# Optimization experiments

Measured on AMD Instinct MI355X. Metric: run time of the kernel, lower is better.

## Reference

```python
import jax, jax.numpy as jnp
import numpy as np

N_STEPS = 20
ALPHA, BETA = 0.9, 0.8  # synaptic / membrane decay (unused given zero carried state, kept for clarity)


def _lcn_spiking_layer(h, knn, w, b):
    """h: [N, d_in]; knn: [d_out, K] indices into d_in; w: [d_out, K]; b: [1, d_out].
    Gather K neighbors per output node, weight, reduce, then snntorch Synaptic
    update with zero carried state (the source never stores returned syn/mem):
      syn = ALPHA*0 + I = I ; reset = (prev_mem > thr) = 0 ; mem = BETA*0 + syn - 0 = I
    and the layer output is mem (the source keeps the 3rd return value)."""
    g = h[:, knn]                                  # [N, d_out, K] irregular gather
    cur = jnp.sum(g * w[None, :, :], axis=2) + b   # [N, d_out]
    syn = ALPHA * jnp.zeros_like(cur) + cur
    mem = BETA * jnp.zeros_like(cur) + syn         # reset term is zero
    return mem


def setup_inputs() -> dict:
    key = jax.random.key(0)
    B, T, IN_DIM, K, OUT = 32, N_STEPS, 14400, 25, 2
    dims = [7200, 3600, 1800, 900, 450]
    ks = jax.random.split(key, 13)
    inp = {"x": jax.random.normal(ks[0], (B, T, IN_DIM), dtype=jnp.float32)}
    prev = IN_DIM
    for i, d in enumerate(dims):
        inp[f"w{i}"] = jax.random.normal(ks[1 + i], (d, K), dtype=jnp.float32) * (2.0 / K) ** 0.5
        inp[f"b{i}"] = jnp.zeros((1, d), dtype=jnp.float32)
        inp[f"knn{i}"] = jax.random.randint(ks[6 + i], (d, K), 0, prev)
        prev = d
    inp["Wfc"] = jax.random.normal(ks[11], (dims[-1], OUT), dtype=jnp.float32) * (1.0 / dims[-1]) ** 0.5
    inp["bfc"] = jnp.zeros((OUT,), dtype=jnp.float32)
    return inp


def reference(x, w0, w1, w2, w3, w4, b0, b1, b2, b3, b4, Wfc, bfc,
              knn0, knn1, knn2, knn3, knn4):
    # Source loops over 20 timesteps with independent (state never carried) work;
    # fold time into batch to vectorize, then keep the last step's angle only,
    # exactly matching the returned value of the torch forward.
    B, T, D = x.shape
    h = x.reshape(B * T, D)
    layers = ((w0, b0, knn0), (w1, b1, knn1), (w2, b2, knn2), (w3, b3, knn3), (w4, b4, knn4))
    for w, b, knn in layers:
        h = _lcn_spiking_layer(h, knn, w, b)
    angle = h @ Wfc + bfc                     # [B*T, out_dim]
    angle = angle.reshape(B, T, -1)[:, -1]    # last timestep, as in the source
    return angle
```

## Files before the change

### kernel.cpp

```cpp
#include <hip/hip_runtime.h>
#include <hip/hip_bf16.h>


#define ROWS 32
#define TSTEPS 20
#define D0 14400
#define D1 7200
#define D2 3600
#define D3 1800
#define D4 900
#define D5 450
#define KNB 25

__global__ __launch_bounds__(256)
void l0_stage(const float* __restrict__ x, float* __restrict__ h1t,
              const float* __restrict__ w, const float* __restrict__ bvec,
              const int* __restrict__ knn)
{
    __shared__ float s[D0];
    const int r = blockIdx.y;
    const float* xrow = x + ((size_t)r * TSTEPS + (TSTEPS - 1)) * (size_t)D0;

    const float4* src = reinterpret_cast<const float4*>(xrow);
    float4* dst = reinterpret_cast<float4*>(s);
#pragma unroll 1
    for (int i = threadIdx.x; i < D0 / 4; i += 256)
        dst[i] = src[i];
    __syncthreads();

    const int j0 = blockIdx.x * 900;
#pragma unroll 1
    for (int j = j0 + threadIdx.x; j < j0 + 900; j += 256) {
        const int*   kn = knn + j * KNB;
        const float* ww = w   + j * KNB;
        float acc = bvec[j];
#pragma unroll
        for (int k = 0; k < KNB; ++k)
            acc += s[kn[k]] * ww[k];
        h1t[(j << 5) + r] = acc;
    }
}

__global__ __launch_bounds__(256)
void layer_t_k(const float* __restrict__ pin, float* __restrict__ pout,
               const float* __restrict__ w, const float* __restrict__ bvec,
               const int* __restrict__ knn, int npairs)
{
    const int lane = threadIdx.x & 63;
    const int r  = lane & 31;
    const int jj = lane >> 5;
    const int nw = gridDim.x << 2;
#pragma unroll 1
    for (int jp = (blockIdx.x << 2) + (threadIdx.x >> 6); jp < npairs; jp += nw) {
        const int j = (jp << 1) + jj;
        const int*   kn = knn + j * KNB;
        const float* ww = w   + j * KNB;
        float acc = bvec[j];
#pragma unroll
        for (int k = 0; k < KNB; ++k)
            acc += pin[(kn[k] << 5) + r] * ww[k];
        pout[(j << 5) + r] = acc;
    }
}

__global__ __launch_bounds__(256)
void l4_fc(const float* __restrict__ h4t,
           const float* __restrict__ w, const float* __restrict__ bvec,
           const int* __restrict__ knn,
           const float* __restrict__ Wfc, const float* __restrict__ bfc,
           float* __restrict__ out)
{
    __shared__ float sacc[64];
    if (threadIdx.x < 64)
        sacc[threadIdx.x] = (blockIdx.x == 0) ? bfc[threadIdx.x & 1] : 0.0f;
    __syncthreads();

    const int lane = threadIdx.x & 63;
    const int r  = lane & 31;
    const int jj = lane >> 5;
    const int nw = gridDim.x << 2;
    float c0 = 0.0f, c1 = 0.0f;
#pragma unroll 1
    for (int jp = (blockIdx.x << 2) + (threadIdx.x >> 6); jp < D5 / 2; jp += nw) {
        const int j = (jp << 1) + jj;
        const int*   kn = knn + j * KNB;
        const float* ww = w   + j * KNB;
        float acc = bvec[j];
#pragma unroll
        for (int k = 0; k < KNB; ++k)
            acc += h4t[(kn[k] << 5) + r] * ww[k];
        c0 += acc * Wfc[j * 2 + 0];
        c1 += acc * Wfc[j * 2 + 1];
    }
    atomicAdd(&sacc[(r << 1) + 0], c0);
    atomicAdd(&sacc[(r << 1) + 1], c1);
    __syncthreads();
    if (threadIdx.x < 64)
        atomicAdd(&out[threadIdx.x], sacc[threadIdx.x]);
}

extern "C" void kernel_launch(void* const* d_in, const int* in_sizes, int n_in,
                              void* d_out, int out_size, void* d_ws, size_t ws_size,
                              hipStream_t stream)
{
    const float* x    = (const float*)d_in[0];
    const float* w0   = (const float*)d_in[1];
    const float* b0   = (const float*)d_in[2];
    const int*   knn0 = (const int*)  d_in[3];
    const float* w1   = (const float*)d_in[4];
    const float* b1   = (const float*)d_in[5];
    const int*   knn1 = (const int*)  d_in[6];
    const float* w2   = (const float*)d_in[7];
    const float* b2   = (const float*)d_in[8];
    const int*   knn2 = (const int*)  d_in[9];
    const float* w3   = (const float*)d_in[10];
    const float* b3   = (const float*)d_in[11];
    const int*   knn3 = (const int*)  d_in[12];
    const float* w4   = (const float*)d_in[13];
    const float* b4   = (const float*)d_in[14];
    const int*   knn4 = (const int*)  d_in[15];
    const float* Wfc  = (const float*)d_in[16];
    const float* bfc  = (const float*)d_in[17];
    float* out = (float*)d_out;

    float* h1t = (float*)d_ws;
    float* h2t = h1t + (size_t)D1 * ROWS;
    float* h3t = h2t + (size_t)D2 * ROWS;
    float* h4t = h3t + (size_t)D3 * ROWS;

    hipMemsetAsync(out, 0, (size_t)out_size * sizeof(float), stream);

    l0_stage<<<dim3(D1 / 900, ROWS), dim3(256), 0, stream>>>(x, h1t, w0, b0, knn0);

    layer_t_k<<<dim3(450), dim3(256), 0, stream>>>(h1t, h2t, w1, b1, knn1, D2 / 2);

    layer_t_k<<<dim3(225), dim3(256), 0, stream>>>(h2t, h3t, w2, b2, knn2, D3 / 2);

    layer_t_k<<<dim3(113), dim3(256), 0, stream>>>(h3t, h4t, w3, b3, knn3, D4 / 2);

    l4_fc<<<dim3(57), dim3(256), 0, stream>>>(h4t, w4, b4, knn4, Wfc, bfc, out);
}
```

Before: 128.7 us.

## Fuse last two LCN layers and FC into one per-row shared-memory kernel

Replaces the layer-3 gather kernel and the layer-4+FC kernel with a single kernel that runs one 1024-thread block per batch row. Each block stages h3 in shared memory, computes layers 3 and 4 from shared memory, and finishes with a wave-reduced FC. This removes the output memset, the global atomics and two launches. The layer-0 stage also moves to 512-thread blocks with 4 blocks per row, which cuts the number of times x is staged into shared memory. The cost is only 32 blocks for the tail, which leaves most of the GPU idle during those layers.

```diff
diff --git a/kernel.cpp b/kernel.cpp
--- a/kernel.cpp
+++ b/kernel.cpp
@@ -12,7 +12,7 @@
 #define D5 450
 #define KNB 25
 
-__global__ __launch_bounds__(256)
+__global__ __launch_bounds__(512)
 void l0_stage(const float* __restrict__ x, float* __restrict__ h1t,
               const float* __restrict__ w, const float* __restrict__ bvec,
               const int* __restrict__ knn)
@@ -24,13 +24,13 @@
     const float4* src = reinterpret_cast<const float4*>(xrow);
     float4* dst = reinterpret_cast<float4*>(s);
 #pragma unroll 1
-    for (int i = threadIdx.x; i < D0 / 4; i += 256)
+    for (int i = threadIdx.x; i < D0 / 4; i += 512)
         dst[i] = src[i];
     __syncthreads();
 
-    const int j0 = blockIdx.x * 900;
+    const int j0 = blockIdx.x * (D1 / 4);
 #pragma unroll 1
-    for (int j = j0 + threadIdx.x; j < j0 + 900; j += 256) {
+    for (int j = j0 + threadIdx.x; j < j0 + D1 / 4; j += 512) {
         const int*   kn = knn + j * KNB;
         const float* ww = w   + j * KNB;
         float acc = bvec[j];
@@ -63,40 +63,61 @@
     }
 }
 
-__global__ __launch_bounds__(256)
-void l4_fc(const float* __restrict__ h4t,
-           const float* __restrict__ w, const float* __restrict__ bvec,
-           const int* __restrict__ knn,
-           const float* __restrict__ Wfc, const float* __restrict__ bfc,
-           float* __restrict__ out)
+__global__ __launch_bounds__(1024)
+void tail32(const float* __restrict__ h3t,
+            const float* __restrict__ w3, const float* __restrict__ b3, const int* __restrict__ knn3,
+            const float* __restrict__ w4, const float* __restrict__ b4, const int* __restrict__ knn4,
+            const float* __restrict__ Wfc, const float* __restrict__ bfc,
+            float* __restrict__ out)
 {
-    __shared__ float sacc[64];
-    if (threadIdx.x < 64)
-        sacc[threadIdx.x] = (blockIdx.x == 0) ? bfc[threadIdx.x & 1] : 0.0f;
+    __shared__ float s3[D3];
+    __shared__ float s4[D4];
+    __shared__ float s5[D5];
+
+    const int r = blockIdx.x;
+
+#pragma unroll 1
+    for (int i = threadIdx.x; i < D3; i += 1024)
+        s3[i] = h3t[(i << 5) + r];
+    __syncthreads();
+
+    if (threadIdx.x < D4) {
+        const int j = threadIdx.x;
+        const int*   kn = knn3 + j * KNB;
+        const float* ww = w3   + j * KNB;
+        float acc = b3[j];
+#pragma unroll
+        for (int k = 0; k < KNB; ++k)
+            acc += s3[kn[k]] * ww[k];
+        s4[j] = acc;
+    }
+    __syncthreads();
+
+    if (threadIdx.x < D5) {
+        const int j = threadIdx.x;
+        const int*   kn = knn4 + j * KNB;
+        const float* ww = w4   + j * KNB;
+        float acc = b4[j];
+#pragma unroll
+        for (int k = 0; k < KNB; ++k)
+            acc += s4[kn[k]] * ww[k];
+        s5[j] = acc;
+    }
     __syncthreads();
 
     const int lane = threadIdx.x & 63;
-    const int r  = lane & 31;
-    const int jj = lane >> 5;
-    const int nw = gridDim.x << 2;
-    float c0 = 0.0f, c1 = 0.0f;
+    const int wid  = threadIdx.x >> 6;
+    if (wid < 2) {
+        float p = 0.0f;
 #pragma unroll 1
-    for (int jp = (blockIdx.x << 2) + (threadIdx.x >> 6); jp < D5 / 2; jp += nw) {
-        const int j = (jp << 1) + jj;
-        const int*   kn = knn + j * KNB;
-        const float* ww = w   + j * KNB;
-        float acc = bvec[j];
+        for (int i = lane; i < D5; i += 64)
+            p += s5[i] * Wfc[i * 2 + wid];
 #pragma unroll
-        for (int k = 0; k < KNB; ++k)
-            acc += h4t[(kn[k] << 5) + r] * ww[k];
-        c0 += acc * Wfc[j * 2 + 0];
-        c1 += acc * Wfc[j * 2 + 1];
+        for (int off = 32; off; off >>= 1)
+            p += __shfl_down(p, off, 64);
+        if (lane == 0)
+            out[r * 2 + wid] = p + bfc[wid];
     }
-    atomicAdd(&sacc[(r << 1) + 0], c0);
-    atomicAdd(&sacc[(r << 1) + 1], c1);
-    __syncthreads();
-    if (threadIdx.x < 64)
-        atomicAdd(&out[threadIdx.x], sacc[threadIdx.x]);
 }
 
 extern "C" void kernel_launch(void* const* d_in, const int* in_sizes, int n_in,
@@ -126,17 +147,13 @@
     float* h1t = (float*)d_ws;
     float* h2t = h1t + (size_t)D1 * ROWS;
     float* h3t = h2t + (size_t)D2 * ROWS;
-    float* h4t = h3t + (size_t)D3 * ROWS;
 
-    hipMemsetAsync(out, 0, (size_t)out_size * sizeof(float), stream);
-
-    l0_stage<<<dim3(D1 / 900, ROWS), dim3(256), 0, stream>>>(x, h1t, w0, b0, knn0);
+    l0_stage<<<dim3(4, ROWS), dim3(512), 0, stream>>>(x, h1t, w0, b0, knn0);
 
     layer_t_k<<<dim3(450), dim3(256), 0, stream>>>(h1t, h2t, w1, b1, knn1, D2 / 2);
 
     layer_t_k<<<dim3(225), dim3(256), 0, stream>>>(h2t, h3t, w2, b2, knn2, D3 / 2);
 
-    layer_t_k<<<dim3(113), dim3(256), 0, stream>>>(h3t, h4t, w3, b3, knn3, D4 / 2);
-
-    l4_fc<<<dim3(57), dim3(256), 0, stream>>>(h4t, w4, b4, knn4, Wfc, bfc, out);
+    tail32<<<dim3(ROWS), dim3(1024), 0, stream>>>(
+        h3t, w3, b3, knn3, w4, b4, knn4, Wfc, bfc, out);
 }
```

Result: slower. 133.5 us (+3.7%).
